# Performance work log

Measured on AMD Instinct MI355X. Metric: run time of the kernel, lower is better.

## Reference

```python
import jax, jax.numpy as jnp
import numpy as np

N, M, K, D = 65536, 131072, 8, 64
TAU = 0.3
EPS = 1e-6

def setup_inputs() -> dict:
    key = jax.random.key(0)
    ks = jax.random.split(key, 16)
    s = 0.05
    return {
        "f_pts": jax.random.normal(ks[0], (N, D), jnp.float32),
        "pts": jax.random.uniform(ks[1], (N, 3), jnp.float32) * 10.0,
        "z_latent": jax.random.normal(ks[2], (M, D), jnp.float32) * 0.1,
        "centers": jax.random.uniform(ks[3], (M, 3), jnp.float32) * 10.0,
        "cand_idx": jax.random.randint(ks[4], (N, K), 0, M),
        "sim_w1": jax.random.normal(ks[5], (2 * D + 3, 64), jnp.float32) * s,
        "sim_b1": jnp.zeros((64,), jnp.float32),
        "sim_w2": jax.random.normal(ks[6], (64, 1), jnp.float32) * s,
        "sim_b2": jnp.zeros((1,), jnp.float32),
        "gate_w1": jax.random.normal(ks[7], (2 * D, D), jnp.float32) * s,
        "gate_b1": jnp.zeros((D,), jnp.float32),
        "gate_w2": jax.random.normal(ks[8], (D, 1), jnp.float32) * s,
        "gate_b2": jnp.zeros((1,), jnp.float32),
        "W_ih": jax.random.normal(ks[9], (3 * D, D), jnp.float32) * s,
        "W_hh": jax.random.normal(ks[10], (3 * D, D), jnp.float32) * s,
        "b_ih": jnp.zeros((3 * D,), jnp.float32),
        "b_hh": jnp.zeros((3 * D,), jnp.float32),
    }

def _forward(f_pts, pts, z_latent, centers, sim_w1, sim_b1, sim_w2, sim_b2,
             gate_w1, gate_b1, gate_w2, gate_b2, W_ih, W_hh, b_ih, b_hh, cand_idx):
    n, k = cand_idx.shape
    m, d = z_latent.shape
    # --- gather voxel latents / centers for each (point, candidate) pair ---
    z_c = z_latent[cand_idx]                         # (N,K,D)
    delta = pts[:, None, :] - centers[cand_idx]      # (N,K,3)
    f_b = jnp.broadcast_to(f_pts[:, None, :], (n, k, d))
    # --- similarity MLP ---
    x = jnp.concatenate([f_b, z_c, delta], axis=-1)  # (N,K,2D+3)
    h = jax.nn.relu(x @ sim_w1 + sim_b1)
    sim = (h @ sim_w2 + sim_b2)[..., 0]              # (N,K)
    # --- low-temperature top-K routing weights over candidates ---
    w = jax.nn.softmax(sim / TAU, axis=-1)           # (N,K)
    # --- scatter weighted point features to voxels ---
    flat_idx = cand_idx.reshape(-1)                  # (N*K,)
    contrib = (w[..., None] * f_pts[:, None, :]).reshape(-1, d)
    msg = jax.ops.segment_sum(contrib, flat_idx, num_segments=m)     # (M,D)
    wsum = jax.ops.segment_sum(w.reshape(-1), flat_idx, num_segments=m)
    msg = msg / (wsum[:, None] + EPS)                # normalized voxel message
    # --- per-voxel gate ---
    g_in = jnp.concatenate([z_latent, msg], axis=-1)
    gate = jax.nn.sigmoid(jax.nn.relu(g_in @ gate_w1 + gate_b1) @ gate_w2 + gate_b2)  # (M,1)
    # --- GRUCell (torch layout: rows ordered r,z,n) ---
    gi = msg @ W_ih.T + b_ih
    gh = z_latent @ W_hh.T + b_hh
    i_r, i_z, i_n = jnp.split(gi, 3, axis=-1)
    h_r, h_z, h_n = jnp.split(gh, 3, axis=-1)
    r = jax.nn.sigmoid(i_r + h_r)
    zg = jax.nn.sigmoid(i_z + h_z)
    nn_ = jnp.tanh(i_n + r * h_n)
    h_new = (1.0 - zg) * nn_ + zg * z_latent
    # gated latent update
    return z_latent + gate * (h_new - z_latent)

def reference(f_pts, pts, z_latent, centers, cand_idx, sim_w1, sim_b1, sim_w2, sim_b2,
              gate_w1, gate_b1, gate_w2, gate_b2, W_ih, W_hh, b_ih, b_hh):
    return _forward(f_pts, pts, z_latent, centers, sim_w1, sim_b1, sim_w2, sim_b2,
                    gate_w1, gate_b1, gate_w2, gate_b2, W_ih, W_hh, b_ih, b_hh, cand_idx)
```

## Files before the change

### kernel.cpp

```cpp
#include <hip/hip_runtime.h>
#include <hip/hip_fp16.h>
#include <math.h>


typedef short bf16x8 __attribute__((ext_vector_type(8)));
typedef unsigned short u16x8 __attribute__((ext_vector_type(8)));
typedef float f32x4 __attribute__((ext_vector_type(4)));
#define MFMA __builtin_amdgcn_mfma_f32_16x16x32_bf16
#define CAP 32

__device__ __forceinline__ short f2bf(float f) {
  unsigned u = __float_as_uint(f);
  unsigned r = (u + 0x7FFFu + ((u >> 16) & 1u)) >> 16;
  return (short)r;
}

__device__ __forceinline__ float bf2f(unsigned short h) {
  return __uint_as_float(((unsigned)h) << 16);
}

__device__ __forceinline__ float sigm(float x) { return 1.0f / (1.0f + __expf(-x)); }

__global__ __launch_bounds__(256) void prep_kernel(
    const float* __restrict__ z, const float* __restrict__ f,
    const float* __restrict__ sim_w1, const float* __restrict__ sim_b1,
    unsigned short* __restrict__ zbf, unsigned short* __restrict__ fbf,
    unsigned short* __restrict__ HB, int* __restrict__ cursor,
    short* __restrict__ bfZ, int M)
{
  long tid = (long)blockIdx.x * 256 + threadIdx.x;
  long nthr = (long)gridDim.x * 256;

  for (long i = tid; i < M; i += nthr) cursor[i] = 0;

  long nz = (long)M * 64;
  for (long i = tid * 8; i < nz; i += nthr * 8) {
    float4 a = *(const float4*)&z[i];
    float4 b4 = *(const float4*)&z[i + 4];
    u16x8 o;
    o[0] = (unsigned short)f2bf(a.x);  o[1] = (unsigned short)f2bf(a.y);
    o[2] = (unsigned short)f2bf(a.z);  o[3] = (unsigned short)f2bf(a.w);
    o[4] = (unsigned short)f2bf(b4.x); o[5] = (unsigned short)f2bf(b4.y);
    o[6] = (unsigned short)f2bf(b4.z); o[7] = (unsigned short)f2bf(b4.w);
    *(u16x8*)&zbf[i] = o;
  }

  if (blockIdx.x == gridDim.x - 1 && threadIdx.x < 64) {
    int lane = threadIdx.x;
    int lr = lane & 15, lg = lane >> 4;
#pragma unroll
    for (int ct = 0; ct < 4; ++ct)
#pragma unroll
      for (int kt = 0; kt < 3; ++kt) {
        bf16x8 b;
#pragma unroll
        for (int e = 0; e < 8; ++e) {
          int k = kt * 32 + lg * 8 + e;
          float v = (k < 67) ? sim_w1[(64 + k) * 64 + ct * 16 + lr] : 0.0f;
          b[e] = f2bf(v);
        }
        *(bf16x8*)&bfZ[(ct * 3 + kt) * 512 + lane * 8] = b;
      }
  }

  if (blockIdx.x < 1024) {
    int wave = blockIdx.x * 4 + (threadIdx.x >> 6);
    int lane = threadIdx.x & 63;
    int lr = lane & 15, lg = lane >> 4;
    int n0 = wave * 16;

    bf16x8 bf[8];
#pragma unroll
    for (int ct = 0; ct < 4; ++ct)
#pragma unroll
      for (int kt = 0; kt < 2; ++kt) {
        bf16x8 bb;
#pragma unroll
        for (int e = 0; e < 8; ++e)
          bb[e] = f2bf(sim_w1[(kt * 32 + lg * 8 + e) * 64 + ct * 16 + lr]);
        bf[ct * 2 + kt] = bb;
      }

    bf16x8 a[2];
#pragma unroll
    for (int kt = 0; kt < 2; ++kt) {
      const float* src = &f[(long)(n0 + lr) * 64 + kt * 32 + lg * 8];
      float4 v0 = *(const float4*)src;
      float4 v1 = *(const float4*)(src + 4);
      bf16x8 t;
      t[0] = f2bf(v0.x); t[1] = f2bf(v0.y); t[2] = f2bf(v0.z); t[3] = f2bf(v0.w);
      t[4] = f2bf(v1.x); t[5] = f2bf(v1.y); t[6] = f2bf(v1.z); t[7] = f2bf(v1.w);
      a[kt] = t;
    }
    *(bf16x8*)&fbf[(long)(n0 + lr) * 64 + lg * 8] = a[0];
    *(bf16x8*)&fbf[(long)(n0 + lr) * 64 + 32 + lg * 8] = a[1];

    f32x4 acc[4] = {{0,0,0,0},{0,0,0,0},{0,0,0,0},{0,0,0,0}};
#pragma unroll
    for (int ct = 0; ct < 4; ++ct) {
      acc[ct] = MFMA(a[0], bf[ct * 2 + 0], acc[ct], 0, 0, 0);
      acc[ct] = MFMA(a[1], bf[ct * 2 + 1], acc[ct], 0, 0, 0);
    }
#pragma unroll
    for (int ct = 0; ct < 4; ++ct) {
      float b1 = sim_b1[ct * 16 + lr];
#pragma unroll
      for (int e = 0; e < 4; ++e)
        HB[(long)(n0 + lg * 4 + e) * 64 + ct * 16 + lr] =
            (unsigned short)f2bf(acc[ct][e] + b1);
    }
  }
}

#define TPW 4
__global__ __launch_bounds__(256) void pair_kernel(
    const float* __restrict__ pts, const unsigned short* __restrict__ zbf,
    const float* __restrict__ centers, const int* __restrict__ cand_idx,
    const float* __restrict__ sim_w2, const short* __restrict__ bfZ,
    const unsigned short* __restrict__ HB,
    int* __restrict__ cursor, unsigned* __restrict__ rec)
{
  int wave = (blockIdx.x * 256 + threadIdx.x) >> 6;
  int lane = threadIdx.x & 63;
  int lr = lane & 15, lg = lane >> 4;

  int call = cand_idx[wave * 64 + lane];
  int slot = atomicAdd(&cursor[call], 1);

  bf16x8 b[12];
#pragma unroll
  for (int i = 0; i < 12; ++i) b[i] = *(const bf16x8*)&bfZ[i * 512 + lane * 8];
  float w2c[4];
#pragma unroll
  for (int ct = 0; ct < 4; ++ct) w2c[ct] = sim_w2[ct * 16 + lr];

  int c0 = __shfl(call, lr, 64);
  bf16x8 a0 = *(const bf16x8*)&zbf[(long)c0 * 64 + lg * 8];
  bf16x8 a1 = *(const bf16x8*)&zbf[(long)c0 * 64 + 32 + lg * 8];
  float cx = 0, cy = 0, cz = 0, px = 0, py = 0, pz = 0;
  if (lg == 0) {
    cx = centers[c0 * 3 + 0]; cy = centers[c0 * 3 + 1]; cz = centers[c0 * 3 + 2];
    int n = wave * TPW * 2 + (lr >> 3);
    px = pts[n * 3 + 0]; py = pts[n * 3 + 1]; pz = pts[n * 3 + 2];
  }
  float hb[4];
  {
    int nrow = wave * TPW * 2 + (lg >> 1);
#pragma unroll
    for (int ct = 0; ct < 4; ++ct)
      hb[ct] = bf2f(HB[(long)nrow * 64 + ct * 16 + lr]);
  }

  float wst[TPW];

#pragma unroll
  for (int t = 0; t < TPW; ++t) {
    int cn = c0; bf16x8 an0 = a0, an1 = a1;
    float cxn = 0, cyn = 0, czn = 0, pxn = 0, pyn = 0, pzn = 0;
    float hbn[4] = {0, 0, 0, 0};
    if (t + 1 < TPW) {
      cn = __shfl(call, (t + 1) * 16 + lr, 64);
      an0 = *(const bf16x8*)&zbf[(long)cn * 64 + lg * 8];
      an1 = *(const bf16x8*)&zbf[(long)cn * 64 + 32 + lg * 8];
      if (lg == 0) {
        cxn = centers[cn * 3 + 0]; cyn = centers[cn * 3 + 1]; czn = centers[cn * 3 + 2];
        int n = (wave * TPW + t + 1) * 2 + (lr >> 3);
        pxn = pts[n * 3 + 0]; pyn = pts[n * 3 + 1]; pzn = pts[n * 3 + 2];
      }
      int nrow = (wave * TPW + t + 1) * 2 + (lg >> 1);
#pragma unroll
      for (int ct = 0; ct < 4; ++ct)
        hbn[ct] = bf2f(HB[(long)nrow * 64 + ct * 16 + lr]);
    }

    bf16x8 ad = {0, 0, 0, 0, 0, 0, 0, 0};
    if (lg == 0) {
      ad[0] = f2bf(px - cx); ad[1] = f2bf(py - cy); ad[2] = f2bf(pz - cz);
    }

    f32x4 acc[4] = {{0,0,0,0},{0,0,0,0},{0,0,0,0},{0,0,0,0}};
#pragma unroll
    for (int ct = 0; ct < 4; ++ct) {
      acc[ct] = MFMA(a0, b[ct * 3 + 0], acc[ct], 0, 0, 0);
      acc[ct] = MFMA(a1, b[ct * 3 + 1], acc[ct], 0, 0, 0);
      acc[ct] = MFMA(ad, b[ct * 3 + 2], acc[ct], 0, 0, 0);
    }

    f32x4 part = {0.f, 0.f, 0.f, 0.f};
#pragma unroll
    for (int ct = 0; ct < 4; ++ct)
#pragma unroll
      for (int e = 0; e < 4; ++e) {
        float u = fmaxf(acc[ct][e] + hb[ct], 0.0f);
        part[e] = fmaf(u, w2c[ct], part[e]);
      }
#pragma unroll
    for (int m = 1; m <= 8; m <<= 1)
#pragma unroll
      for (int e = 0; e < 4; ++e) part[e] += __shfl_xor(part[e], m, 64);

    float other[4];
#pragma unroll
    for (int e = 0; e < 4; ++e) other[e] = __shfl_xor(part[e], 16, 64);

    float mx = part[0];
#pragma unroll
    for (int e = 1; e < 4; ++e) mx = fmaxf(mx, part[e]);
#pragma unroll
    for (int e = 0; e < 4; ++e) mx = fmaxf(mx, other[e]);
    float ex[4], se = 0.f, so = 0.f;
#pragma unroll
    for (int e = 0; e < 4; ++e) {
      ex[e] = __expf((part[e] - mx) * (1.0f / 0.3f));
      se += ex[e];
      so += __expf((other[e] - mx) * (1.0f / 0.3f));
    }
    float inv = 1.0f / (se + so);

    int srcl = (lane >> 2) << 4;
    float t0 = __shfl(ex[0] * inv, srcl, 64);
    float t1 = __shfl(ex[1] * inv, srcl, 64);
    float t2 = __shfl(ex[2] * inv, srcl, 64);
    float t3 = __shfl(ex[3] * inv, srcl, 64);
    int esel = lane & 3;
    wst[t] = esel == 0 ? t0 : esel == 1 ? t1 : esel == 2 ? t2 : t3;

    c0 = cn; a0 = an0; a1 = an1;
    cx = cxn; cy = cyn; cz = czn; px = pxn; py = pyn; pz = pzn;
#pragma unroll
    for (int ct = 0; ct < 4; ++ct) hb[ct] = hbn[ct];
  }

  float v0 = __shfl(wst[0], lr, 64);
  float v1 = __shfl(wst[1], lr, 64);
  float v2 = __shfl(wst[2], lr, 64);
  float v3 = __shfl(wst[3], lr, 64);
  float wv = lg == 0 ? v0 : lg == 1 ? v1 : lg == 2 ? v2 : v3;

  if (slot < CAP) {
    int n_pt = wave * 8 + 2 * lg + ((lane >> 3) & 1);
    unsigned short wh = __half_as_ushort(__float2half(wv));
    rec[(long)call * CAP + slot] = ((unsigned)n_pt << 16) | (unsigned)wh;
  }
}

__global__ __launch_bounds__(256) void gather_kernel(
    const unsigned* __restrict__ rec, const int* __restrict__ cursor,
    const unsigned short* __restrict__ fbf, unsigned short* __restrict__ msg_bf,
    int mvox)
{
  int tid = blockIdx.x * 256 + threadIdx.x;
  int row = tid >> 2, seg = tid & 3;
  if (row >= mvox) return;

  int cnt = cursor[row];
  cnt = cnt < CAP ? cnt : CAP;
  const unsigned* rp = &rec[(long)row * CAP];

  float acc[16];
#pragma unroll
  for (int j = 0; j < 16; ++j) acc[j] = 0.f;
  float ws = 0.f;

  for (int i = 0; i < cnt; ++i) {
    unsigned r = rp[i];
    float w = __half2float(__ushort_as_half((unsigned short)(r & 0xffffu)));
    int n = r >> 16;
    ws += w;
    const u16x8* fp = (const u16x8*)&fbf[(long)n * 64 + seg * 16];
    u16x8 f0 = fp[0], f1 = fp[1];
#pragma unroll
    for (int j = 0; j < 8; ++j) {
      acc[j]     = fmaf(w, bf2f(f0[j]), acc[j]);
      acc[8 + j] = fmaf(w, bf2f(f1[j]), acc[8 + j]);
    }
  }
  float inv = 1.0f / (ws + 1e-6f);
  u16x8 o0, o1;
#pragma unroll
  for (int j = 0; j < 8; ++j) {
    o0[j] = (unsigned short)f2bf(acc[j] * inv);
    o1[j] = (unsigned short)f2bf(acc[8 + j] * inv);
  }
  *(u16x8*)&msg_bf[(long)row * 64 + seg * 16] = o0;
  *(u16x8*)&msg_bf[(long)row * 64 + seg * 16 + 8] = o1;
}

#define AST 136
#define GST 136
#define WST 88

__global__ __launch_bounds__(512) void stage2(
    const float* __restrict__ z_latent,
    const float* __restrict__ gate_w1, const float* __restrict__ gate_b1,
    const float* __restrict__ gate_w2, const float* __restrict__ gate_b2,
    const float* __restrict__ W_ih, const float* __restrict__ W_hh,
    const float* __restrict__ b_ih, const float* __restrict__ b_hh,
    const unsigned short* __restrict__ msg_bf,
    float* __restrict__ out, int ntiles)
{
  __shared__ short Ab[128 * AST];
  __shared__ short G1t[64 * GST];
  __shared__ short Wih_l[192 * WST];
  __shared__ short Whh_l[192 * WST];
  __shared__ float gb1s[64], gw2s[64], bihs[192], bhhs[192];
  __shared__ float gb2s;

  int t = threadIdx.x;
  for (int s = t; s < 64 * 128; s += 512) {
    int j = s & 63, k = s >> 6;
    G1t[j * GST + k] = f2bf(gate_w1[s]);
  }
  for (int s = t; s < 192 * 64; s += 512) {
    int j = s >> 6, k = s & 63;
    Wih_l[j * WST + k] = f2bf(W_ih[s]);
    Whh_l[j * WST + k] = f2bf(W_hh[s]);
  }
  if (t < 64) { gb1s[t] = gate_b1[t]; gw2s[t] = gate_w2[t]; }
  if (t < 192) { bihs[t] = b_ih[t]; bhhs[t] = b_hh[t]; }
  if (t == 0) gb2s = gate_b2[0];
  __syncthreads();

  int wid = t >> 6, lane = t & 63;
  int lr = lane & 15, lg = lane >> 4;

  for (int tile = blockIdx.x; tile < ntiles; tile += gridDim.x) {
    int r0 = tile * 128;
    {
      int row = t >> 2, seg = t & 3;
      const float4* zp = (const float4*)&z_latent[(long)(r0 + row) * 64 + seg * 16];
      const u16x8* mp = (const u16x8*)&msg_bf[(long)(r0 + row) * 64 + seg * 16];
      short* az = &Ab[row * AST + seg * 16];
      short* am = &Ab[row * AST + 64 + seg * 16];
#pragma unroll
      for (int q = 0; q < 4; ++q) {
        float4 zv = zp[q];
        az[q * 4 + 0] = f2bf(zv.x); az[q * 4 + 1] = f2bf(zv.y);
        az[q * 4 + 2] = f2bf(zv.z); az[q * 4 + 3] = f2bf(zv.w);
      }
      *(u16x8*)&am[0] = mp[0];
      *(u16x8*)&am[8] = mp[1];
    }
    __syncthreads();

    int rowbase = r0 + wid * 16;
    bf16x8 a[4];
#pragma unroll
    for (int kt = 0; kt < 4; ++kt)
      a[kt] = *(const bf16x8*)&Ab[(wid * 16 + lr) * AST + kt * 32 + lg * 8];

    f32x4 hnew[4], zs[4];
    f32x4 usum = {0.f, 0.f, 0.f, 0.f};

#pragma unroll
    for (int ct = 0; ct < 4; ++ct) {
      f32x4 au = {0,0,0,0}, air = {0,0,0,0}, aiz = {0,0,0,0}, ain = {0,0,0,0};
      f32x4 ahr = {0,0,0,0}, ahz = {0,0,0,0}, ahn = {0,0,0,0};
#pragma unroll
      for (int kt = 0; kt < 4; ++kt)
        au = MFMA(a[kt], *(const bf16x8*)&G1t[(ct * 16 + lr) * GST + kt * 32 + lg * 8], au, 0, 0, 0);
#pragma unroll
      for (int k2 = 0; k2 < 2; ++k2) {
        bf16x8 amg = a[2 + k2];
        bf16x8 az_ = a[k2];
        int ko = k2 * 32 + lg * 8;
        air = MFMA(amg, *(const bf16x8*)&Wih_l[(      ct * 16 + lr) * WST + ko], air, 0, 0, 0);
        aiz = MFMA(amg, *(const bf16x8*)&Wih_l[( 64 + ct * 16 + lr) * WST + ko], aiz, 0, 0, 0);
        ain = MFMA(amg, *(const bf16x8*)&Wih_l[(128 + ct * 16 + lr) * WST + ko], ain, 0, 0, 0);
        ahr = MFMA(az_, *(const bf16x8*)&Whh_l[(      ct * 16 + lr) * WST + ko], ahr, 0, 0, 0);
        ahz = MFMA(az_, *(const bf16x8*)&Whh_l[( 64 + ct * 16 + lr) * WST + ko], ahz, 0, 0, 0);
        ahn = MFMA(az_, *(const bf16x8*)&Whh_l[(128 + ct * 16 + lr) * WST + ko], ahn, 0, 0, 0);
      }
      int c = ct * 16 + lr;
#pragma unroll
      for (int e = 0; e < 4; ++e) {
        float zv = z_latent[(long)(rowbase + lg * 4 + e) * 64 + c];
        zs[ct][e] = zv;
        float uu = fmaxf(au[e] + gb1s[c], 0.0f);
        usum[e] += uu * gw2s[c];
        float rr = sigm(air[e] + bihs[c] + ahr[e] + bhhs[c]);
        float zg = sigm(aiz[e] + bihs[64 + c] + ahz[e] + bhhs[64 + c]);
        float nn = tanhf(ain[e] + bihs[128 + c] + rr * (ahn[e] + bhhs[128 + c]));
        hnew[ct][e] = (1.0f - zg) * nn + zg * zv;
      }
    }

#pragma unroll
    for (int m = 1; m <= 8; m <<= 1)
#pragma unroll
      for (int e = 0; e < 4; ++e) {
        float v = usum[e];
        usum[e] = v + __shfl_xor(v, m, 64);
      }
    float gate[4];
#pragma unroll
    for (int e = 0; e < 4; ++e) gate[e] = sigm(usum[e] + gb2s);

#pragma unroll
    for (int ct = 0; ct < 4; ++ct)
#pragma unroll
      for (int e = 0; e < 4; ++e)
        out[(long)(rowbase + lg * 4 + e) * 64 + ct * 16 + lr] =
            zs[ct][e] + gate[e] * (hnew[ct][e] - zs[ct][e]);
    __syncthreads();
  }
}

extern "C" void kernel_launch(void* const* d_in, const int* in_sizes, int n_in,
                              void* d_out, int out_size, void* d_ws, size_t ws_size,
                              hipStream_t stream) {
  const float* f_pts   = (const float*)d_in[0];
  const float* pts     = (const float*)d_in[1];
  const float* z_lat   = (const float*)d_in[2];
  const float* centers = (const float*)d_in[3];
  const int*   cand    = (const int*)d_in[4];
  const float* sim_w1  = (const float*)d_in[5];
  const float* sim_b1  = (const float*)d_in[6];
  const float* sim_w2  = (const float*)d_in[7];
  const float* gate_w1 = (const float*)d_in[9];
  const float* gate_b1 = (const float*)d_in[10];
  const float* gate_w2 = (const float*)d_in[11];
  const float* gate_b2 = (const float*)d_in[12];
  const float* W_ih    = (const float*)d_in[13];
  const float* W_hh    = (const float*)d_in[14];
  const float* b_ih    = (const float*)d_in[15];
  const float* b_hh    = (const float*)d_in[16];

  int N = in_sizes[0] / 64;
  int M = in_sizes[2] / 64;

  int* cursor = (int*)d_ws;
  unsigned* rec = (unsigned*)(cursor + M);
  unsigned short* zbf = (unsigned short*)(rec + (size_t)M * CAP);
  unsigned short* msg_bf = zbf;
  unsigned short* fbf = zbf + (size_t)M * 64;
  unsigned short* HB = fbf + (size_t)N * 64;
  short* bfZ = (short*)(HB + (size_t)N * 64);

  prep_kernel<<<2048, 256, 0, stream>>>(z_lat, f_pts, sim_w1, sim_b1,
                                        zbf, fbf, HB, cursor, bfZ, M);

  pair_kernel<<<2048, 256, 0, stream>>>(pts, zbf, centers, cand,
                                        sim_w2, bfZ, HB, cursor, rec);

  gather_kernel<<<(M * 4) / 256, 256, 0, stream>>>(rec, cursor, fbf, msg_bf, M);

  int ntiles = M / 128;
  stage2<<<256, 512, 0, stream>>>(z_lat, gate_w1, gate_b1, gate_w2, gate_b2,
                                  W_ih, W_hh, b_ih, b_hh, msg_bf,
                                  (float*)d_out, ntiles);
}
```

Before: 109.5 us.

## Pack hidden bias, double pair work per wave, stream stage2 from bf16

The sim-MLP first-layer bias/product buffer is now stored so each lane's four channels sit together, letting pair_kernel fetch them with one 8-byte load. Each pair_kernel wave now handles twice as many point-candidate tiles (TPW 8), with two candidate indices and atomics per lane. gather_kernel reads its records four at a time as uint4. stage2 drops the shared-memory staging tile and reads bf16 z and messages directly, with the grid and occupancy raised. The message buffer now reuses the record buffer, and the final blend uses bf16-rounded z instead of fp32 z, which risks accuracy and an in-place read/write hazard.

Measured after the change: 331.8 us. 203% more time.

```diff
diff --git a/kernel.cpp b/kernel.cpp
--- a/kernel.cpp
+++ b/kernel.cpp
@@ -25,7 +25,7 @@
     const float* __restrict__ z, const float* __restrict__ f,
     const float* __restrict__ sim_w1, const float* __restrict__ sim_b1,
     unsigned short* __restrict__ zbf, unsigned short* __restrict__ fbf,
-    unsigned short* __restrict__ HB, int* __restrict__ cursor,
+    unsigned short* __restrict__ HBt, int* __restrict__ cursor,
     short* __restrict__ bfZ, int M)
 {
   long tid = (long)blockIdx.x * 256 + threadIdx.x;
@@ -101,31 +101,35 @@
       acc[ct] = MFMA(a[0], bf[ct * 2 + 0], acc[ct], 0, 0, 0);
       acc[ct] = MFMA(a[1], bf[ct * 2 + 1], acc[ct], 0, 0, 0);
     }
-#pragma unroll
-    for (int ct = 0; ct < 4; ++ct) {
-      float b1 = sim_b1[ct * 16 + lr];
-#pragma unroll
-      for (int e = 0; e < 4; ++e)
-        HB[(long)(n0 + lg * 4 + e) * 64 + ct * 16 + lr] =
-            (unsigned short)f2bf(acc[ct][e] + b1);
-    }
-  }
-}
-
-#define TPW 4
+    float b10 = sim_b1[lr], b11 = sim_b1[16 + lr];
+    float b12 = sim_b1[32 + lr], b13 = sim_b1[48 + lr];
+#pragma unroll
+    for (int e = 0; e < 4; ++e) {
+      unsigned lo = (unsigned)(unsigned short)f2bf(acc[0][e] + b10)
+                  | ((unsigned)(unsigned short)f2bf(acc[1][e] + b11) << 16);
+      unsigned hi = (unsigned)(unsigned short)f2bf(acc[2][e] + b12)
+                  | ((unsigned)(unsigned short)f2bf(acc[3][e] + b13) << 16);
+      *(uint2*)&HBt[(long)(n0 + lg * 4 + e) * 64 + lr * 4] = make_uint2(lo, hi);
+    }
+  }
+}
+
+#define TPW 8
 __global__ __launch_bounds__(256) void pair_kernel(
     const float* __restrict__ pts, const unsigned short* __restrict__ zbf,
     const float* __restrict__ centers, const int* __restrict__ cand_idx,
     const float* __restrict__ sim_w2, const short* __restrict__ bfZ,
-    const unsigned short* __restrict__ HB,
+    const unsigned short* __restrict__ HBt,
     int* __restrict__ cursor, unsigned* __restrict__ rec)
 {
   int wave = (blockIdx.x * 256 + threadIdx.x) >> 6;
   int lane = threadIdx.x & 63;
   int lr = lane & 15, lg = lane >> 4;
 
-  int call = cand_idx[wave * 64 + lane];
-  int slot = atomicAdd(&cursor[call], 1);
+  int callA = cand_idx[wave * 128 + lane];
+  int callB = cand_idx[wave * 128 + 64 + lane];
+  int slotA = atomicAdd(&cursor[callA], 1);
+  int slotB = atomicAdd(&cursor[callB], 1);
 
   bf16x8 b[12];
 #pragma unroll
@@ -134,7 +138,7 @@
 #pragma unroll
   for (int ct = 0; ct < 4; ++ct) w2c[ct] = sim_w2[ct * 16 + lr];
 
-  int c0 = __shfl(call, lr, 64);
+  int c0 = __shfl(callA, lr, 64);
   bf16x8 a0 = *(const bf16x8*)&zbf[(long)c0 * 64 + lg * 8];
   bf16x8 a1 = *(const bf16x8*)&zbf[(long)c0 * 64 + 32 + lg * 8];
   float cx = 0, cy = 0, cz = 0, px = 0, py = 0, pz = 0;
@@ -143,13 +147,7 @@
     int n = wave * TPW * 2 + (lr >> 3);
     px = pts[n * 3 + 0]; py = pts[n * 3 + 1]; pz = pts[n * 3 + 2];
   }
-  float hb[4];
-  {
-    int nrow = wave * TPW * 2 + (lg >> 1);
-#pragma unroll
-    for (int ct = 0; ct < 4; ++ct)
-      hb[ct] = bf2f(HB[(long)nrow * 64 + ct * 16 + lr]);
-  }
+  uint2 h2 = *(const uint2*)&HBt[((long)wave * TPW * 2 + (lg >> 1)) * 64 + lr * 4];
 
   float wst[TPW];
 
@@ -157,9 +155,9 @@
   for (int t = 0; t < TPW; ++t) {
     int cn = c0; bf16x8 an0 = a0, an1 = a1;
     float cxn = 0, cyn = 0, czn = 0, pxn = 0, pyn = 0, pzn = 0;
-    float hbn[4] = {0, 0, 0, 0};
+    uint2 h2n = make_uint2(0, 0);
     if (t + 1 < TPW) {
-      cn = __shfl(call, (t + 1) * 16 + lr, 64);
+      cn = __shfl((t + 1) < 4 ? callA : callB, ((t + 1) & 3) * 16 + lr, 64);
       an0 = *(const bf16x8*)&zbf[(long)cn * 64 + lg * 8];
       an1 = *(const bf16x8*)&zbf[(long)cn * 64 + 32 + lg * 8];
       if (lg == 0) {
@@ -167,10 +165,7 @@
         int n = (wave * TPW + t + 1) * 2 + (lr >> 3);
         pxn = pts[n * 3 + 0]; pyn = pts[n * 3 + 1]; pzn = pts[n * 3 + 2];
       }
-      int nrow = (wave * TPW + t + 1) * 2 + (lg >> 1);
-#pragma unroll
-      for (int ct = 0; ct < 4; ++ct)
-        hbn[ct] = bf2f(HB[(long)nrow * 64 + ct * 16 + lr]);
+      h2n = *(const uint2*)&HBt[((long)(wave * TPW + t + 1) * 2 + (lg >> 1)) * 64 + lr * 4];
     }
 
     bf16x8 ad = {0, 0, 0, 0, 0, 0, 0, 0};
@@ -185,6 +180,12 @@
       acc[ct] = MFMA(a1, b[ct * 3 + 1], acc[ct], 0, 0, 0);
       acc[ct] = MFMA(ad, b[ct * 3 + 2], acc[ct], 0, 0, 0);
     }
+
+    float hb[4];
+    hb[0] = bf2f((unsigned short)(h2.x));
+    hb[1] = bf2f((unsigned short)(h2.x >> 16));
+    hb[2] = bf2f((unsigned short)(h2.y));
+    hb[3] = bf2f((unsigned short)(h2.y >> 16));
 
     f32x4 part = {0.f, 0.f, 0.f, 0.f};
 #pragma unroll
@@ -227,20 +228,28 @@
 
     c0 = cn; a0 = an0; a1 = an1;
     cx = cxn; cy = cyn; cz = czn; px = pxn; py = pyn; pz = pzn;
-#pragma unroll
-    for (int ct = 0; ct < 4; ++ct) hb[ct] = hbn[ct];
+    h2 = h2n;
   }
 
   float v0 = __shfl(wst[0], lr, 64);
   float v1 = __shfl(wst[1], lr, 64);
   float v2 = __shfl(wst[2], lr, 64);
   float v3 = __shfl(wst[3], lr, 64);
-  float wv = lg == 0 ? v0 : lg == 1 ? v1 : lg == 2 ? v2 : v3;
-
-  if (slot < CAP) {
-    int n_pt = wave * 8 + 2 * lg + ((lane >> 3) & 1);
-    unsigned short wh = __half_as_ushort(__float2half(wv));
-    rec[(long)call * CAP + slot] = ((unsigned)n_pt << 16) | (unsigned)wh;
+  float v4 = __shfl(wst[4], lr, 64);
+  float v5 = __shfl(wst[5], lr, 64);
+  float v6 = __shfl(wst[6], lr, 64);
+  float v7 = __shfl(wst[7], lr, 64);
+  float wvA = lg == 0 ? v0 : lg == 1 ? v1 : lg == 2 ? v2 : v3;
+  float wvB = lg == 0 ? v4 : lg == 1 ? v5 : lg == 2 ? v6 : v7;
+
+  int base_pt = wave * 16 + 2 * lg + (lr >> 3);
+  if (slotA < CAP) {
+    unsigned short wh = __half_as_ushort(__float2half(wvA));
+    rec[(long)callA * CAP + slotA] = ((unsigned)base_pt << 16) | (unsigned)wh;
+  }
+  if (slotB < CAP) {
+    unsigned short wh = __half_as_ushort(__float2half(wvB));
+    rec[(long)callB * CAP + slotB] = ((unsigned)(base_pt + 8) << 16) | (unsigned)wh;
   }
 }
 
@@ -262,17 +271,24 @@
   for (int j = 0; j < 16; ++j) acc[j] = 0.f;
   float ws = 0.f;
 
-  for (int i = 0; i < cnt; ++i) {
-    unsigned r = rp[i];
-    float w = __half2float(__ushort_as_half((unsigned short)(r & 0xffffu)));
-    int n = r >> 16;
-    ws += w;
-    const u16x8* fp = (const u16x8*)&fbf[(long)n * 64 + seg * 16];
-    u16x8 f0 = fp[0], f1 = fp[1];
-#pragma unroll
-    for (int j = 0; j < 8; ++j) {
-      acc[j]     = fmaf(w, bf2f(f0[j]), acc[j]);
-      acc[8 + j] = fmaf(w, bf2f(f1[j]), acc[8 + j]);
+  for (int i0 = 0; i0 < cnt; i0 += 4) {
+    uint4 r4 = *(const uint4*)&rp[i0];
+    unsigned rr0 = r4.x, rr1 = r4.y, rr2 = r4.z, rr3 = r4.w;
+#pragma unroll
+    for (int j = 0; j < 4; ++j) {
+      unsigned r = j == 0 ? rr0 : j == 1 ? rr1 : j == 2 ? rr2 : rr3;
+      if (i0 + j < cnt) {
+        float w = __half2float(__ushort_as_half((unsigned short)(r & 0xffffu)));
+        int n = r >> 16;
+        ws += w;
+        const u16x8* fp = (const u16x8*)&fbf[(long)n * 64 + seg * 16];
+        u16x8 f0 = fp[0], f1 = fp[1];
+#pragma unroll
+        for (int k = 0; k < 8; ++k) {
+          acc[k]     = fmaf(w, bf2f(f0[k]), acc[k]);
+          acc[8 + k] = fmaf(w, bf2f(f1[k]), acc[8 + k]);
+        }
+      }
     }
   }
   float inv = 1.0f / (ws + 1e-6f);
@@ -286,12 +302,11 @@
   *(u16x8*)&msg_bf[(long)row * 64 + seg * 16 + 8] = o1;
 }
 
-#define AST 136
 #define GST 136
-#define WST 88
-
-__global__ __launch_bounds__(512) void stage2(
-    const float* __restrict__ z_latent,
+#define WST 72
+
+__global__ __launch_bounds__(512, 4) void stage2(
+    const unsigned short* __restrict__ zbf,
     const float* __restrict__ gate_w1, const float* __restrict__ gate_b1,
     const float* __restrict__ gate_w2, const float* __restrict__ gate_b2,
     const float* __restrict__ W_ih, const float* __restrict__ W_hh,
@@ -299,7 +314,6 @@
     const unsigned short* __restrict__ msg_bf,
     float* __restrict__ out, int ntiles)
 {
-  __shared__ short Ab[128 * AST];
   __shared__ short G1t[64 * GST];
   __shared__ short Wih_l[192 * WST];
   __shared__ short Whh_l[192 * WST];
@@ -325,29 +339,13 @@
   int lr = lane & 15, lg = lane >> 4;
 
   for (int tile = blockIdx.x; tile < ntiles; tile += gridDim.x) {
-    int r0 = tile * 128;
-    {
-      int row = t >> 2, seg = t & 3;
-      const float4* zp = (const float4*)&z_latent[(long)(r0 + row) * 64 + seg * 16];
-      const u16x8* mp = (const u16x8*)&msg_bf[(long)(r0 + row) * 64 + seg * 16];
-      short* az = &Ab[row * AST + seg * 16];
-      short* am = &Ab[row * AST + 64 + seg * 16];
-#pragma unroll
-      for (int q = 0; q < 4; ++q) {
-        float4 zv = zp[q];
-        az[q * 4 + 0] = f2bf(zv.x); az[q * 4 + 1] = f2bf(zv.y);
-        az[q * 4 + 2] = f2bf(zv.z); az[q * 4 + 3] = f2bf(zv.w);
-      }
-      *(u16x8*)&am[0] = mp[0];
-      *(u16x8*)&am[8] = mp[1];
-    }
-    __syncthreads();
-
-    int rowbase = r0 + wid * 16;
+    int rowbase = tile * 128 + wid * 16;
+    long abase = (long)(rowbase + lr) * 64;
     bf16x8 a[4];
-#pragma unroll
-    for (int kt = 0; kt < 4; ++kt)
-      a[kt] = *(const bf16x8*)&Ab[(wid * 16 + lr) * AST + kt * 32 + lg * 8];
+    a[0] = *(const bf16x8*)&zbf[abase + lg * 8];
+    a[1] = *(const bf16x8*)&zbf[abase + 32 + lg * 8];
+    a[2] = *(const bf16x8*)&msg_bf[abase + lg * 8];
+    a[3] = *(const bf16x8*)&msg_bf[abase + 32 + lg * 8];
 
     f32x4 hnew[4], zs[4];
     f32x4 usum = {0.f, 0.f, 0.f, 0.f};
@@ -374,7 +372,7 @@
       int c = ct * 16 + lr;
 #pragma unroll
       for (int e = 0; e < 4; ++e) {
-        float zv = z_latent[(long)(rowbase + lg * 4 + e) * 64 + c];
+        float zv = bf2f(zbf[(long)(rowbase + lg * 4 + e) * 64 + c]);
         zs[ct][e] = zv;
         float uu = fmaxf(au[e] + gb1s[c], 0.0f);
         usum[e] += uu * gw2s[c];
@@ -402,7 +400,6 @@
       for (int e = 0; e < 4; ++e)
         out[(long)(rowbase + lg * 4 + e) * 64 + ct * 16 + lr] =
             zs[ct][e] + gate[e] * (hnew[ct][e] - zs[ct][e]);
-    __syncthreads();
   }
 }
 
@@ -431,22 +428,23 @@
 
   int* cursor = (int*)d_ws;
   unsigned* rec = (unsigned*)(cursor + M);
+  unsigned short* msg_bf = (unsigned short*)rec;
   unsigned short* zbf = (unsigned short*)(rec + (size_t)M * CAP);
-  unsigned short* msg_bf = zbf;
   unsigned short* fbf = zbf + (size_t)M * 64;
-  unsigned short* HB = fbf + (size_t)N * 64;
-  short* bfZ = (short*)(HB + (size_t)N * 64);
+  unsigned short* HBt = fbf + (size_t)N * 64;
+  short* bfZ = (short*)(HBt + (size_t)N * 64);
 
   prep_kernel<<<2048, 256, 0, stream>>>(z_lat, f_pts, sim_w1, sim_b1,
-                                        zbf, fbf, HB, cursor, bfZ, M);
-
-  pair_kernel<<<2048, 256, 0, stream>>>(pts, zbf, centers, cand,
-                                        sim_w2, bfZ, HB, cursor, rec);
+                                        zbf, fbf, HBt, cursor, bfZ, M);
+
+  int nwaves = (N * 8) / (16 * TPW);
+  pair_kernel<<<nwaves / 4, 256, 0, stream>>>(pts, zbf, centers, cand,
+                                              sim_w2, bfZ, HBt, cursor, rec);
 
   gather_kernel<<<(M * 4) / 256, 256, 0, stream>>>(rec, cursor, fbf, msg_bf, M);
 
   int ntiles = M / 128;
-  stage2<<<256, 512, 0, stream>>>(z_lat, gate_w1, gate_b1, gate_w2, gate_b2,
+  stage2<<<512, 512, 0, stream>>>(zbf, gate_w1, gate_b1, gate_w2, gate_b2,
                                   W_ih, W_hh, b_ih, b_hh, msg_bf,
                                   (float*)d_out, ntiles);
 }
```
